# Optimization experiments

Measured on AMD Instinct MI355X. Metric: run time of the kernel, lower is better.

The kernel has to match this reference:

```python
import jax, jax.numpy as jnp
import numpy as np

NUM_CLASSES = 19
MIN_SAMPLES = 1000.0
LOSS_WEIGHT = 1.0
TWO_PI = 2.0 * np.pi


def _nearest_upsample(x, H, W):
    # x: [D, h, w] -> [D, H, W]; matches torch F.interpolate(mode='nearest')
    h, w = x.shape[1], x.shape[2]
    ih = jnp.arange(H) * h // H
    iw = jnp.arange(W) * w // W
    return x[:, ih][:, :, iw]


def _smooth_l1(a, b):
    # F.smooth_l1_loss with beta=1.0, mean reduction
    d = jnp.abs(a - b)
    return jnp.mean(jnp.where(d < 1.0, 0.5 * d * d, d - 0.5))


def setup_inputs() -> dict:
    key = jax.random.key(0)
    k1, k2 = jax.random.split(key)
    feature = jax.random.normal(k1, (1, 64, 128, 128), dtype=jnp.float32)
    label = jax.random.randint(k2, (1, 1, 512, 512), 0, NUM_CLASSES)
    return {"feature": feature, "label": label}


def reference(feature, label):
    D = feature.shape[1]
    H, W = label.shape[2], label.shape[3]
    feat = _nearest_upsample(feature[0], H, W).reshape(D, -1)   # [D, P]
    lab = label[0, 0].reshape(-1)                               # [P]
    ks = jnp.arange(-3, 4, dtype=feat.dtype)                    # 7 gaussian bins

    def per_class(c):
        mask = (lab == c).astype(feat.dtype)                    # [P]
        n = jnp.sum(mask)
        n_safe = jnp.maximum(n, 1.0)
        miu = (feat * mask).sum(1) / n_safe                     # [D]
        var = (((feat - miu[:, None]) ** 2) * mask).sum(1) / n_safe + 1e-10
        std = jnp.sqrt(var)
        var_s = var / 25.0
        bins = miu[:, None] + ks[None, :] * std[:, None]        # [D, 7]
        # KDE: sum over class pixels of N(bin; feat_p, var_s), vectorized over bins
        z2 = (bins[:, :, None] - feat[:, None, :]) ** 2 / var_s[:, None, None]  # [D,7,P]
        sample_values = (jnp.exp(-0.5 * z2) * mask[None, None, :]).sum(-1) / jnp.sqrt(TWO_PI * var_s)[:, None]
        # target computed under no_grad in the original: bin - miu = k*std
        target_values = jax.lax.stop_gradient(
            jnp.exp(-0.5 * ks ** 2)[None, :] / jnp.sqrt(TWO_PI * var)[:, None]
        )
        hist = sample_values / jnp.maximum(sample_values.sum(1, keepdims=True), 1e-30)
        targ = target_values / target_values.sum(1, keepdims=True)
        active = (n >= MIN_SAMPLES).astype(feat.dtype)
        return _smooth_l1(hist, targ) * active, active

    losses, actives = jax.lax.map(per_class, jnp.arange(NUM_CLASSES))
    return LOSS_WEIGHT * jnp.sum(losses) / jnp.sum(actives)
```

## Files before the change

### kernel.cpp

```cpp
#include <hip/hip_runtime.h>
#include <hip/hip_bf16.h>

#define SRC    16384
#define DCH    64
#define NCLS   19
#define NPAIR  (NCLS*DCH)

__device__ __forceinline__ float exp2_raw(float x)
{
    float r;
    asm("v_exp_f32 %0, %1" : "=v"(r) : "v"(x));
    return r;
}

__global__ __launch_bounds__(256) void hl_count_kernel(
    const int* __restrict__ label, unsigned char* __restrict__ cnt,
    float* __restrict__ psum)
{
    if (blockIdx.x == 0 && threadIdx.x == 0) psum[0] = 0.f;
    int s  = blockIdx.x * 256 + threadIdx.x;
    int sy = s >> 7, sx = s & 127;
    const int4* lab4 = (const int4*)label;
    int l[16];
#pragma unroll
    for (int r = 0; r < 4; r++) {
        int4 v = lab4[(4 * sy + r) * 128 + sx];
        l[4 * r + 0] = v.x; l[4 * r + 1] = v.y;
        l[4 * r + 2] = v.z; l[4 * r + 3] = v.w;
    }
#pragma unroll
    for (int c = 0; c < NCLS; c++) {
        int cc = 0;
#pragma unroll
        for (int j = 0; j < 16; j++) cc += (l[j] == c) ? 1 : 0;
        cnt[c * SRC + s] = (unsigned char)cc;
    }
}

__global__ __launch_bounds__(256, 4) void hl_fused_kernel(
    const float* __restrict__ feature, const unsigned char* __restrict__ cnt,
    int* __restrict__ ncls, float* __restrict__ psum)
{
    int w = blockIdx.x;
    int c = w >> 6, d = w & 63;
    int t = threadIdx.x;
    int wid = t >> 6;

    const float4*       fp4 = (const float4*)(feature + d * SRC);
    const unsigned int* cpu = (const unsigned int*)(cnt + c * SRC);

    float f1 = 0.f, f2 = 0.f;
    int   nc = 0;
#pragma unroll 4
    for (int i = 0; i < 16; i++) {
        int g = i * 256 + t;
        float4       x  = fp4[g];
        unsigned int cv = cpu[g];
        float xs[4] = {x.x, x.y, x.z, x.w};
        float cf[4] = {(float)(cv & 255u), (float)((cv >> 8) & 255u),
                       (float)((cv >> 16) & 255u), (float)(cv >> 24)};
#pragma unroll
        for (int e = 0; e < 4; e++) {
            float wx = cf[e] * xs[e];
            f1 += wx;
            f2 = fmaf(wx, xs[e], f2);
        }
        nc += (cv & 255u) + ((cv >> 8) & 255u) + ((cv >> 16) & 255u) + (cv >> 24);
    }
    double s1 = (double)f1, s2 = (double)f2;
#pragma unroll
    for (int o = 32; o > 0; o >>= 1) {
        s1 += __shfl_down(s1, o);
        s2 += __shfl_down(s2, o);
        nc += __shfl_down(nc, o);
    }
    __shared__ double ps1[4], ps2[4];
    __shared__ int    pn[4];
    __shared__ float  sh_mu, sh_istd;
    __shared__ int    sh_act;
    if ((t & 63) == 0) { ps1[wid] = s1; ps2[wid] = s2; pn[wid] = nc; }
    __syncthreads();
    if (t == 0) {
        double a = ps1[0] + ps1[1] + ps1[2] + ps1[3];
        double b = ps2[0] + ps2[1] + ps2[2] + ps2[3];
        int    n = pn[0] + pn[1] + pn[2] + pn[3];
        double nsafe = (n > 0) ? (double)n : 1.0;
        double mu  = a / nsafe;
        double var = (b - 2.0 * mu * a + mu * mu * (double)n) / nsafe + 1e-10;
        sh_mu   = (float)mu;
        sh_istd = (float)(1.0 / sqrt(var));
        sh_act  = (n >= 1000);
        if (d == 0) ncls[c] = n;
    }
    __syncthreads();
    if (!sh_act) return;
    float istd = sh_istd;
    float nm   = -sh_mu * istd;

    const float C1 = -18.033688011112042f;
    float acc[7] = {0.f, 0.f, 0.f, 0.f, 0.f, 0.f, 0.f};

#pragma unroll 2
    for (int i = 0; i < 16; i++) {
        int g = i * 256 + t;
        float4       x  = fp4[g];
        unsigned int cv = cpu[g];
        float xs[4] = {x.x, x.y, x.z, x.w};
        float cf[4] = {(float)(cv & 255u), (float)((cv >> 8) & 255u),
                       (float)((cv >> 16) & 255u), (float)(cv >> 24)};
#pragma unroll
        for (int e = 0; e < 4; e++) {
            float u = fmaf(xs[e], istd, nm);
            float p = C1 * u;
            float q = p * u;
#pragma unroll
            for (int k = 0; k < 7; k++) {
                float km  = (float)(k - 3);
                float arg = fmaf(p, -2.f * km, q + C1 * km * km);
                acc[k] = fmaf(cf[e], exp2_raw(arg), acc[k]);
            }
        }
    }

    __shared__ float part[4][7];
#pragma unroll
    for (int j = 0; j < 7; j++) {
        float v = acc[j];
#pragma unroll
        for (int o = 32; o > 0; o >>= 1) v += __shfl_down(v, o);
        if ((t & 63) == 0) part[wid][j] = v;
    }
    __syncthreads();

    if (t == 0) {
        double e[7], z = 0.0;
#pragma unroll
        for (int k = -3; k <= 3; k++) { e[k + 3] = exp(-0.5 * (double)(k * k)); z += e[k + 3]; }

        float hist[7], S = 0.f;
#pragma unroll
        for (int j = 0; j < 7; j++) {
            hist[j] = part[0][j] + part[1][j] + part[2][j] + part[3][j];
            S += hist[j];
        }
        float Ss = fmaxf(S, 1e-30f);
        float ps = 0.f;
#pragma unroll
        for (int j = 0; j < 7; j++) {
            float dd = fabsf(hist[j] / Ss - (float)(e[j] / z));
            ps += (dd < 1.f) ? 0.5f * dd * dd : (dd - 0.5f);
        }
        atomicAdd(psum, ps);
    }
}

__global__ __launch_bounds__(64) void hl_final_kernel(
    const float* __restrict__ psum, const int* __restrict__ ncls,
    float* __restrict__ out)
{
    if (threadIdx.x == 0) {
        int A = 0;
#pragma unroll
        for (int i = 0; i < NCLS; i++) A += (ncls[i] >= 1000) ? 1 : 0;
        out[0] = (A > 0) ? psum[0] / (448.0f * (float)A) : 0.0f;
    }
}

extern "C" void kernel_launch(void* const* d_in, const int* in_sizes, int n_in,
                              void* d_out, int out_size, void* d_ws, size_t ws_size,
                              hipStream_t stream)
{
    const float* feature = (const float*)d_in[0];
    const int*   label   = (const int*)d_in[1];
    float*       out     = (float*)d_out;

    char* ws = (char*)d_ws;
    unsigned char* cnt  = (unsigned char*)(ws);
    int*           ncls = (int*)(ws + 311296);
    float*         psum = (float*)(ws + 311424);

    hl_count_kernel<<<SRC / 256, 256, 0, stream>>>(label, cnt, psum);
    hl_fused_kernel<<<NPAIR, 256, 0, stream>>>(feature, cnt, ncls, psum);
    hl_final_kernel<<<1, 64, 0, stream>>>(psum, ncls, out);
}
```

Measured before the change: 88.75 us.

## Compact nonzero class-pixel entries and split moments/KDE into sliced kernels

Replaces the dense per-class count map with a compacted list of (pixel, count) entries per class, built with ballot/atomic stream compaction. The moments and KDE passes become separate kernels that each split a class-channel pair over four slices and iterate only over pixels that contain the class. This avoids exp work on zero-weight pixels and raises block parallelism. In exchange it reads features through gathers and adds launches plus a workspace reduction of partial moments and bins.

Measured after the change: 105.7 us. 19.1% more time.

```diff
diff --git a/kernel.cpp b/kernel.cpp
--- a/kernel.cpp
+++ b/kernel.cpp
@@ -1,10 +1,10 @@
 #include <hip/hip_runtime.h>
-#include <hip/hip_bf16.h>
 
 #define SRC    16384
 #define DCH    64
 #define NCLS   19
 #define NPAIR  (NCLS*DCH)
+#define SLICES 4
 
 __device__ __forceinline__ float exp2_raw(float x)
 {
@@ -13,12 +13,17 @@
     return r;
 }
 
-__global__ __launch_bounds__(256) void hl_count_kernel(
-    const int* __restrict__ label, unsigned char* __restrict__ cnt,
-    float* __restrict__ psum)
-{
-    if (blockIdx.x == 0 && threadIdx.x == 0) psum[0] = 0.f;
-    int s  = blockIdx.x * 256 + threadIdx.x;
+__global__ __launch_bounds__(64) void hl_zero_kernel(unsigned int* __restrict__ nnz)
+{
+    if (threadIdx.x < NCLS) nnz[threadIdx.x] = 0u;
+}
+
+__global__ __launch_bounds__(256) void hl_count_compact(
+    const int* __restrict__ label, unsigned int* __restrict__ entries,
+    unsigned int* __restrict__ nnz)
+{
+    int t = threadIdx.x;
+    int s = blockIdx.x * 256 + t;
     int sy = s >> 7, sx = s & 127;
     const int4* lab4 = (const int4*)label;
     int l[16];
@@ -28,101 +33,157 @@
         l[4 * r + 0] = v.x; l[4 * r + 1] = v.y;
         l[4 * r + 2] = v.z; l[4 * r + 3] = v.w;
     }
+    int cc[NCLS];
 #pragma unroll
     for (int c = 0; c < NCLS; c++) {
-        int cc = 0;
-#pragma unroll
-        for (int j = 0; j < 16; j++) cc += (l[j] == c) ? 1 : 0;
-        cnt[c * SRC + s] = (unsigned char)cc;
-    }
-}
-
-__global__ __launch_bounds__(256, 4) void hl_fused_kernel(
-    const float* __restrict__ feature, const unsigned char* __restrict__ cnt,
-    int* __restrict__ ncls, float* __restrict__ psum)
-{
-    int w = blockIdx.x;
-    int c = w >> 6, d = w & 63;
-    int t = threadIdx.x;
-    int wid = t >> 6;
-
-    const float4*       fp4 = (const float4*)(feature + d * SRC);
-    const unsigned int* cpu = (const unsigned int*)(cnt + c * SRC);
+        int n = 0;
+#pragma unroll
+        for (int j = 0; j < 16; j++) n += (l[j] == c) ? 1 : 0;
+        cc[c] = n;
+    }
+
+    __shared__ int wcnt[NCLS][4];
+    __shared__ int sbase[NCLS][4];
+    int lane = t & 63, wid = t >> 6;
+    unsigned long long lt = (1ULL << lane) - 1ULL;
+
+#pragma unroll
+    for (int c = 0; c < NCLS; c++) {
+        unsigned long long m = __ballot(cc[c] > 0);
+        if (lane == 0) wcnt[c][wid] = __popcll(m);
+    }
+    __syncthreads();
+    if (t < NCLS) {
+        int a0 = wcnt[t][0], a1 = wcnt[t][1], a2 = wcnt[t][2], a3 = wcnt[t][3];
+        unsigned int base = atomicAdd(&nnz[t], (unsigned int)(a0 + a1 + a2 + a3));
+        sbase[t][0] = (int)base;
+        sbase[t][1] = (int)base + a0;
+        sbase[t][2] = (int)base + a0 + a1;
+        sbase[t][3] = (int)base + a0 + a1 + a2;
+    }
+    __syncthreads();
+#pragma unroll
+    for (int c = 0; c < NCLS; c++) {
+        unsigned long long m = __ballot(cc[c] > 0);
+        int rank = __popcll(m & lt);
+        if (cc[c] > 0)
+            entries[c * SRC + sbase[c][wid] + rank] =
+                (unsigned int)s | ((unsigned int)cc[c] << 14);
+    }
+}
+
+__global__ __launch_bounds__(256, 4) void hl_moments(
+    const float* __restrict__ feature, const unsigned int* __restrict__ entries,
+    const unsigned int* __restrict__ nnz,
+    double* __restrict__ ms1, double* __restrict__ ms2,
+    unsigned int* __restrict__ mn)
+{
+    int bx = blockIdx.x;
+    int pair = bx >> 2, slice = bx & 3;
+    int c = pair >> 6, d = pair & 63;
+    int t = threadIdx.x;
+
+    int nz  = (int)nnz[c];
+    int per = (nz + SLICES - 1) >> 2;
+    int jb  = slice * per;
+    int j1  = min(jb + per, nz);
+    const unsigned int* lst = entries + c * SRC;
+    const float*        fd  = feature + d * SRC;
 
     float f1 = 0.f, f2 = 0.f;
-    int   nc = 0;
-#pragma unroll 4
-    for (int i = 0; i < 16; i++) {
-        int g = i * 256 + t;
-        float4       x  = fp4[g];
-        unsigned int cv = cpu[g];
-        float xs[4] = {x.x, x.y, x.z, x.w};
-        float cf[4] = {(float)(cv & 255u), (float)((cv >> 8) & 255u),
-                       (float)((cv >> 16) & 255u), (float)(cv >> 24)};
-#pragma unroll
-        for (int e = 0; e < 4; e++) {
-            float wx = cf[e] * xs[e];
-            f1 += wx;
-            f2 = fmaf(wx, xs[e], f2);
-        }
-        nc += (cv & 255u) + ((cv >> 8) & 255u) + ((cv >> 16) & 255u) + (cv >> 24);
+    unsigned int ncnt = 0;
+    for (int j = jb + t; j < j1; j += 256) {
+        unsigned int e  = lst[j];
+        float        x  = fd[e & 16383u];
+        unsigned int cu = e >> 14;
+        float        cf = (float)cu;
+        float        wx = cf * x;
+        f1 += wx;
+        f2 = fmaf(wx, x, f2);
+        ncnt += cu;
     }
     double s1 = (double)f1, s2 = (double)f2;
 #pragma unroll
     for (int o = 32; o > 0; o >>= 1) {
         s1 += __shfl_down(s1, o);
         s2 += __shfl_down(s2, o);
-        nc += __shfl_down(nc, o);
-    }
-    __shared__ double ps1[4], ps2[4];
-    __shared__ int    pn[4];
-    __shared__ float  sh_mu, sh_istd;
-    __shared__ int    sh_act;
-    if ((t & 63) == 0) { ps1[wid] = s1; ps2[wid] = s2; pn[wid] = nc; }
+        ncnt += __shfl_down(ncnt, o);
+    }
+    __shared__ double       p1[4], p2[4];
+    __shared__ unsigned int pn[4];
+    int wid = t >> 6;
+    if ((t & 63) == 0) { p1[wid] = s1; p2[wid] = s2; pn[wid] = ncnt; }
     __syncthreads();
     if (t == 0) {
-        double a = ps1[0] + ps1[1] + ps1[2] + ps1[3];
-        double b = ps2[0] + ps2[1] + ps2[2] + ps2[3];
-        int    n = pn[0] + pn[1] + pn[2] + pn[3];
+        int idx = pair * SLICES + slice;
+        ms1[idx] = p1[0] + p1[1] + p1[2] + p1[3];
+        ms2[idx] = p2[0] + p2[1] + p2[2] + p2[3];
+        mn[idx]  = pn[0] + pn[1] + pn[2] + pn[3];
+    }
+}
+
+__global__ __launch_bounds__(256, 4) void hl_kde(
+    const float* __restrict__ feature, const unsigned int* __restrict__ entries,
+    const unsigned int* __restrict__ nnz,
+    const double* __restrict__ ms1, const double* __restrict__ ms2,
+    const unsigned int* __restrict__ mn, float* __restrict__ bins)
+{
+    int bx = blockIdx.x;
+    int pair = bx >> 2, slice = bx & 3;
+    int c = pair >> 6, d = pair & 63;
+    int t = threadIdx.x;
+
+    __shared__ float sh_istd, sh_nm;
+    __shared__ int   sh_act;
+    if (t == 0) {
+        int base = pair * SLICES;
+        unsigned int n = mn[base] + mn[base + 1] + mn[base + 2] + mn[base + 3];
+        double a = ms1[base] + ms1[base + 1] + ms1[base + 2] + ms1[base + 3];
+        double b = ms2[base] + ms2[base + 1] + ms2[base + 2] + ms2[base + 3];
         double nsafe = (n > 0) ? (double)n : 1.0;
         double mu  = a / nsafe;
         double var = (b - 2.0 * mu * a + mu * mu * (double)n) / nsafe + 1e-10;
-        sh_mu   = (float)mu;
-        sh_istd = (float)(1.0 / sqrt(var));
+        float istd = (float)(1.0 / sqrt(var));
+        sh_istd = istd;
+        sh_nm   = -(float)mu * istd;
         sh_act  = (n >= 1000);
-        if (d == 0) ncls[c] = n;
     }
     __syncthreads();
     if (!sh_act) return;
-    float istd = sh_istd;
-    float nm   = -sh_mu * istd;
+    float istd = sh_istd, nm = sh_nm;
+
+    int nz  = (int)nnz[c];
+    int per = (nz + SLICES - 1) >> 2;
+    int jb  = slice * per;
+    int j1  = min(jb + per, nz);
+    const unsigned int* lst = entries + c * SRC;
+    const float*        fd  = feature + d * SRC;
 
     const float C1 = -18.033688011112042f;
     float acc[7] = {0.f, 0.f, 0.f, 0.f, 0.f, 0.f, 0.f};
 
 #pragma unroll 2
-    for (int i = 0; i < 16; i++) {
-        int g = i * 256 + t;
-        float4       x  = fp4[g];
-        unsigned int cv = cpu[g];
-        float xs[4] = {x.x, x.y, x.z, x.w};
-        float cf[4] = {(float)(cv & 255u), (float)((cv >> 8) & 255u),
-                       (float)((cv >> 16) & 255u), (float)(cv >> 24)};
-#pragma unroll
-        for (int e = 0; e < 4; e++) {
-            float u = fmaf(xs[e], istd, nm);
-            float p = C1 * u;
-            float q = p * u;
-#pragma unroll
-            for (int k = 0; k < 7; k++) {
-                float km  = (float)(k - 3);
-                float arg = fmaf(p, -2.f * km, q + C1 * km * km);
-                acc[k] = fmaf(cf[e], exp2_raw(arg), acc[k]);
-            }
-        }
+    for (int j = jb + t; j < j1; j += 256) {
+        unsigned int e = lst[j];
+        float x  = fd[e & 16383u];
+        float cf = (float)(e >> 14);
+        float u  = fmaf(x, istd, nm);
+        float p  = C1 * u;
+        float q  = p * u;
+        float t1 = q + C1;
+        float t4 = q + 4.f * C1;
+        float t9 = q + 9.f * C1;
+        acc[0] = fmaf(cf, exp2_raw(fmaf(p,  6.f, t9)), acc[0]);
+        acc[1] = fmaf(cf, exp2_raw(fmaf(p,  4.f, t4)), acc[1]);
+        acc[2] = fmaf(cf, exp2_raw(fmaf(p,  2.f, t1)), acc[2]);
+        acc[3] = fmaf(cf, exp2_raw(q),                 acc[3]);
+        acc[4] = fmaf(cf, exp2_raw(fmaf(p, -2.f, t1)), acc[4]);
+        acc[5] = fmaf(cf, exp2_raw(fmaf(p, -4.f, t4)), acc[5]);
+        acc[6] = fmaf(cf, exp2_raw(fmaf(p, -6.f, t9)), acc[6]);
     }
 
     __shared__ float part[4][7];
+    int wid = t >> 6;
 #pragma unroll
     for (int j = 0; j < 7; j++) {
         float v = acc[j];
@@ -131,38 +192,61 @@
         if ((t & 63) == 0) part[wid][j] = v;
     }
     __syncthreads();
-
-    if (t == 0) {
-        double e[7], z = 0.0;
-#pragma unroll
-        for (int k = -3; k <= 3; k++) { e[k + 3] = exp(-0.5 * (double)(k * k)); z += e[k + 3]; }
-
-        float hist[7], S = 0.f;
+    if (t < 7)
+        bins[(pair * SLICES + slice) * 7 + t] =
+            part[0][t] + part[1][t] + part[2][t] + part[3][t];
+}
+
+__global__ __launch_bounds__(256) void hl_final_kernel(
+    const float* __restrict__ bins, const unsigned int* __restrict__ mn,
+    float* __restrict__ out)
+{
+    int t = threadIdx.x;
+    double e[7], z = 0.0;
+#pragma unroll
+    for (int k = -3; k <= 3; k++) { e[k + 3] = exp(-0.5 * (double)(k * k)); z += e[k + 3]; }
+    float tg[7];
+#pragma unroll
+    for (int j = 0; j < 7; j++) tg[j] = (float)(e[j] / z);
+
+    float tot = 0.f;
+    for (int pair = t; pair < NPAIR; pair += 256) {
+        int c  = pair >> 6;
+        int nb = (c << 6) * SLICES;
+        unsigned int n = mn[nb] + mn[nb + 1] + mn[nb + 2] + mn[nb + 3];
+        if (n < 1000) continue;
+        float h[7], S = 0.f;
 #pragma unroll
         for (int j = 0; j < 7; j++) {
-            hist[j] = part[0][j] + part[1][j] + part[2][j] + part[3][j];
-            S += hist[j];
+            int bb = pair * (SLICES * 7) + j;
+            h[j] = bins[bb] + bins[bb + 7] + bins[bb + 14] + bins[bb + 21];
+            S += h[j];
         }
         float Ss = fmaxf(S, 1e-30f);
         float ps = 0.f;
 #pragma unroll
         for (int j = 0; j < 7; j++) {
-            float dd = fabsf(hist[j] / Ss - (float)(e[j] / z));
+            float dd = fabsf(h[j] / Ss - tg[j]);
             ps += (dd < 1.f) ? 0.5f * dd * dd : (dd - 0.5f);
         }
-        atomicAdd(psum, ps);
-    }
-}
-
-__global__ __launch_bounds__(64) void hl_final_kernel(
-    const float* __restrict__ psum, const int* __restrict__ ncls,
-    float* __restrict__ out)
-{
-    if (threadIdx.x == 0) {
+        tot += ps;
+    }
+#pragma unroll
+    for (int o = 32; o > 0; o >>= 1) tot += __shfl_down(tot, o);
+    __shared__ float pr[4];
+    int wid = t >> 6;
+    if ((t & 63) == 0) pr[wid] = tot;
+    __syncthreads();
+    if (t == 0) {
+        float T = pr[0] + pr[1] + pr[2] + pr[3];
         int A = 0;
 #pragma unroll
-        for (int i = 0; i < NCLS; i++) A += (ncls[i] >= 1000) ? 1 : 0;
-        out[0] = (A > 0) ? psum[0] / (448.0f * (float)A) : 0.0f;
+        for (int c = 0; c < NCLS; c++) {
+            int nb = (c << 6) * SLICES;
+            unsigned int n = mn[nb] + mn[nb + 1] + mn[nb + 2] + mn[nb + 3];
+            A += (n >= 1000) ? 1 : 0;
+        }
+        out[0] = (A > 0) ? T / (448.0f * (float)A) : 0.0f;
     }
 }
 
@@ -175,11 +259,16 @@
     float*       out     = (float*)d_out;
 
     char* ws = (char*)d_ws;
-    unsigned char* cnt  = (unsigned char*)(ws);
-    int*           ncls = (int*)(ws + 311296);
-    float*         psum = (float*)(ws + 311424);
-
-    hl_count_kernel<<<SRC / 256, 256, 0, stream>>>(label, cnt, psum);
-    hl_fused_kernel<<<NPAIR, 256, 0, stream>>>(feature, cnt, ncls, psum);
-    hl_final_kernel<<<1, 64, 0, stream>>>(psum, ncls, out);
-}
+    unsigned int* entries = (unsigned int*)(ws);
+    double*       ms1     = (double*)(ws + 1245184);
+    double*       ms2     = (double*)(ws + 1284096);
+    unsigned int* mn      = (unsigned int*)(ws + 1323008);
+    float*        bins    = (float*)(ws + 1342464);
+    unsigned int* nnz     = (unsigned int*)(ws + 1478656);
+
+    hl_zero_kernel<<<1, 64, 0, stream>>>(nnz);
+    hl_count_compact<<<SRC / 256, 256, 0, stream>>>(label, entries, nnz);
+    hl_moments<<<NPAIR * SLICES, 256, 0, stream>>>(feature, entries, nnz, ms1, ms2, mn);
+    hl_kde<<<NPAIR * SLICES, 256, 0, stream>>>(feature, entries, nnz, ms1, ms2, mn, bins);
+    hl_final_kernel<<<1, 256, 0, stream>>>(bins, mn, out);
+}
```

## Split fused kernel into moments and sliced KDE kernels with deterministic final reduce

Applied to the files above, without the earlier changes.

The fused per-(class,channel) kernel is split into a moments kernel and a KDE kernel whose grid is four times larger, each block handling a quarter of the pixels. Partial bin sums go to a workspace array and are combined in a single-block final kernel, replacing the float atomicAdd. The KDE inner loop also hoists the per-bin constant terms. This is meant to improve occupancy and load balance in the exp-heavy phase, at the cost of an extra launch, re-reading feature/cnt data, and a serial final reduction.

Result: slower. 102.8 us (+15.9%).

```diff
diff --git a/kernel.cpp b/kernel.cpp
--- a/kernel.cpp
+++ b/kernel.cpp
@@ -1,10 +1,10 @@
 #include <hip/hip_runtime.h>
-#include <hip/hip_bf16.h>
 
 #define SRC    16384
 #define DCH    64
 #define NCLS   19
 #define NPAIR  (NCLS*DCH)
+#define KSL    4
 
 __device__ __forceinline__ float exp2_raw(float x)
 {
@@ -14,10 +14,8 @@
 }
 
 __global__ __launch_bounds__(256) void hl_count_kernel(
-    const int* __restrict__ label, unsigned char* __restrict__ cnt,
-    float* __restrict__ psum)
-{
-    if (blockIdx.x == 0 && threadIdx.x == 0) psum[0] = 0.f;
+    const int* __restrict__ label, unsigned char* __restrict__ cnt)
+{
     int s  = blockIdx.x * 256 + threadIdx.x;
     int sy = s >> 7, sx = s & 127;
     const int4* lab4 = (const int4*)label;
@@ -37,9 +35,9 @@
     }
 }
 
-__global__ __launch_bounds__(256, 4) void hl_fused_kernel(
+__global__ __launch_bounds__(256, 4) void hl_moments(
     const float* __restrict__ feature, const unsigned char* __restrict__ cnt,
-    int* __restrict__ ncls, float* __restrict__ psum)
+    float4* __restrict__ minfo, unsigned int* __restrict__ ncls)
 {
     int w = blockIdx.x;
     int c = w >> 6, d = w & 63;
@@ -76,8 +74,6 @@
     }
     __shared__ double ps1[4], ps2[4];
     __shared__ int    pn[4];
-    __shared__ float  sh_mu, sh_istd;
-    __shared__ int    sh_act;
     if ((t & 63) == 0) { ps1[wid] = s1; ps2[wid] = s2; pn[wid] = nc; }
     __syncthreads();
     if (t == 0) {
@@ -87,22 +83,40 @@
         double nsafe = (n > 0) ? (double)n : 1.0;
         double mu  = a / nsafe;
         double var = (b - 2.0 * mu * a + mu * mu * (double)n) / nsafe + 1e-10;
-        sh_mu   = (float)mu;
-        sh_istd = (float)(1.0 / sqrt(var));
-        sh_act  = (n >= 1000);
-        if (d == 0) ncls[c] = n;
-    }
-    __syncthreads();
-    if (!sh_act) return;
-    float istd = sh_istd;
-    float nm   = -sh_mu * istd;
+        float istd = (float)(1.0 / sqrt(var));
+        float muf  = (float)mu;
+        float4 mi;
+        mi.x = istd;
+        mi.y = -muf * istd;
+        mi.z = (n >= 1000) ? 1.0f : 0.0f;
+        mi.w = 0.f;
+        minfo[w] = mi;
+        if (d == 0) ncls[c] = (unsigned int)n;
+    }
+}
+
+__global__ __launch_bounds__(256, 4) void hl_kde(
+    const float* __restrict__ feature, const unsigned char* __restrict__ cnt,
+    const float4* __restrict__ minfo, float* __restrict__ bins)
+{
+    int bx = blockIdx.x;
+    int pair = bx >> 2, slice = bx & 3;
+    int c = pair >> 6, d = pair & 63;
+    int t = threadIdx.x;
+
+    float4 mi = minfo[pair];
+    if (mi.z == 0.0f) return;
+    float istd = mi.x, nm = mi.y;
+
+    const float4*       fp4 = (const float4*)(feature + d * SRC);
+    const unsigned int* cpu = (const unsigned int*)(cnt + c * SRC);
 
     const float C1 = -18.033688011112042f;
     float acc[7] = {0.f, 0.f, 0.f, 0.f, 0.f, 0.f, 0.f};
 
-#pragma unroll 2
-    for (int i = 0; i < 16; i++) {
-        int g = i * 256 + t;
+#pragma unroll
+    for (int i = 0; i < 4; i++) {
+        int g = slice * 1024 + i * 256 + t;
         float4       x  = fp4[g];
         unsigned int cv = cpu[g];
         float xs[4] = {x.x, x.y, x.z, x.w};
@@ -110,19 +124,24 @@
                        (float)((cv >> 16) & 255u), (float)(cv >> 24)};
 #pragma unroll
         for (int e = 0; e < 4; e++) {
-            float u = fmaf(xs[e], istd, nm);
-            float p = C1 * u;
-            float q = p * u;
-#pragma unroll
-            for (int k = 0; k < 7; k++) {
-                float km  = (float)(k - 3);
-                float arg = fmaf(p, -2.f * km, q + C1 * km * km);
-                acc[k] = fmaf(cf[e], exp2_raw(arg), acc[k]);
-            }
+            float u  = fmaf(xs[e], istd, nm);
+            float p  = C1 * u;
+            float q  = p * u;
+            float t1 = q + C1;
+            float t4 = q + 4.f * C1;
+            float t9 = q + 9.f * C1;
+            acc[0] = fmaf(cf[e], exp2_raw(fmaf(p,  6.f, t9)), acc[0]);
+            acc[1] = fmaf(cf[e], exp2_raw(fmaf(p,  4.f, t4)), acc[1]);
+            acc[2] = fmaf(cf[e], exp2_raw(fmaf(p,  2.f, t1)), acc[2]);
+            acc[3] = fmaf(cf[e], exp2_raw(q),                 acc[3]);
+            acc[4] = fmaf(cf[e], exp2_raw(fmaf(p, -2.f, t1)), acc[4]);
+            acc[5] = fmaf(cf[e], exp2_raw(fmaf(p, -4.f, t4)), acc[5]);
+            acc[6] = fmaf(cf[e], exp2_raw(fmaf(p, -6.f, t9)), acc[6]);
         }
     }
 
     __shared__ float part[4][7];
+    int wid = t >> 6;
 #pragma unroll
     for (int j = 0; j < 7; j++) {
         float v = acc[j];
@@ -131,38 +150,54 @@
         if ((t & 63) == 0) part[wid][j] = v;
     }
     __syncthreads();
-
-    if (t == 0) {
-        double e[7], z = 0.0;
-#pragma unroll
-        for (int k = -3; k <= 3; k++) { e[k + 3] = exp(-0.5 * (double)(k * k)); z += e[k + 3]; }
-
-        float hist[7], S = 0.f;
+    if (t < 7)
+        bins[bx * 7 + t] = part[0][t] + part[1][t] + part[2][t] + part[3][t];
+}
+
+__global__ __launch_bounds__(256) void hl_final_kernel(
+    const float* __restrict__ bins, const unsigned int* __restrict__ ncls,
+    float* __restrict__ out)
+{
+    int t = threadIdx.x;
+    double e[7], z = 0.0;
+#pragma unroll
+    for (int k = -3; k <= 3; k++) { e[k + 3] = exp(-0.5 * (double)(k * k)); z += e[k + 3]; }
+    float tg[7];
+#pragma unroll
+    for (int j = 0; j < 7; j++) tg[j] = (float)(e[j] / z);
+
+    float tot = 0.f;
+    for (int pair = t; pair < NPAIR; pair += 256) {
+        int c = pair >> 6;
+        if (ncls[c] < 1000u) continue;
+        float h[7], S = 0.f;
 #pragma unroll
         for (int j = 0; j < 7; j++) {
-            hist[j] = part[0][j] + part[1][j] + part[2][j] + part[3][j];
-            S += hist[j];
+            int bb = pair * (KSL * 7) + j;
+            h[j] = bins[bb] + bins[bb + 7] + bins[bb + 14] + bins[bb + 21];
+            S += h[j];
         }
         float Ss = fmaxf(S, 1e-30f);
         float ps = 0.f;
 #pragma unroll
         for (int j = 0; j < 7; j++) {
-            float dd = fabsf(hist[j] / Ss - (float)(e[j] / z));
+            float dd = fabsf(h[j] / Ss - tg[j]);
             ps += (dd < 1.f) ? 0.5f * dd * dd : (dd - 0.5f);
         }
-        atomicAdd(psum, ps);
-    }
-}
-
-__global__ __launch_bounds__(64) void hl_final_kernel(
-    const float* __restrict__ psum, const int* __restrict__ ncls,
-    float* __restrict__ out)
-{
-    if (threadIdx.x == 0) {
+        tot += ps;
+    }
+#pragma unroll
+    for (int o = 32; o > 0; o >>= 1) tot += __shfl_down(tot, o);
+    __shared__ float pr[4];
+    int wid = t >> 6;
+    if ((t & 63) == 0) pr[wid] = tot;
+    __syncthreads();
+    if (t == 0) {
+        float T = pr[0] + pr[1] + pr[2] + pr[3];
         int A = 0;
 #pragma unroll
-        for (int i = 0; i < NCLS; i++) A += (ncls[i] >= 1000) ? 1 : 0;
-        out[0] = (A > 0) ? psum[0] / (448.0f * (float)A) : 0.0f;
+        for (int c = 0; c < NCLS; c++) A += (ncls[c] >= 1000u) ? 1 : 0;
+        out[0] = (A > 0) ? T / (448.0f * (float)A) : 0.0f;
     }
 }
 
@@ -175,11 +210,13 @@
     float*       out     = (float*)d_out;
 
     char* ws = (char*)d_ws;
-    unsigned char* cnt  = (unsigned char*)(ws);
-    int*           ncls = (int*)(ws + 311296);
-    float*         psum = (float*)(ws + 311424);
-
-    hl_count_kernel<<<SRC / 256, 256, 0, stream>>>(label, cnt, psum);
-    hl_fused_kernel<<<NPAIR, 256, 0, stream>>>(feature, cnt, ncls, psum);
-    hl_final_kernel<<<1, 64, 0, stream>>>(psum, ncls, out);
-}
+    unsigned char* cnt   = (unsigned char*)(ws);
+    float4*        minfo = (float4*)(ws + 311296);
+    unsigned int*  ncls  = (unsigned int*)(ws + 330752);
+    float*         bins  = (float*)(ws + 330880);
+
+    hl_count_kernel<<<SRC / 256, 256, 0, stream>>>(label, cnt);
+    hl_moments<<<NPAIR, 256, 0, stream>>>(feature, cnt, minfo, ncls);
+    hl_kde<<<NPAIR * KSL, 256, 0, stream>>>(feature, cnt, minfo, bins);
+    hl_final_kernel<<<1, 256, 0, stream>>>(bins, ncls, out);
+}
```
